# Kernel tuning notes

Measured on AMD Instinct MI355X. Metric: run time of the kernel, lower is better.

The kernel has to match this reference:

```python
import jax, jax.numpy as jnp
import numpy as np

E = 2048  # embed_size == seq_len (required: edge_weight_fc maps last dim E -> 1 on the NxN scores)
B = 4
N = 2048


def setup_inputs() -> dict:
    key = jax.random.key(0)
    ks = jax.random.split(key, 12)
    s = 0.02
    inp = {
        "query": jax.random.normal(ks[0], (B, N, E), jnp.float32),
        "key": jax.random.normal(ks[1], (B, N, E), jnp.float32),
        "value": jax.random.normal(ks[2], (B, N, E), jnp.float32),
        "mask": jax.random.randint(ks[3], (B, N, N), 0, 2, jnp.int32),
        # nn.Linear weights stored torch-style as [out, in]
        "Wq": jax.random.normal(ks[4], (E, E), jnp.float32) * s,
        "bq": jnp.zeros((E,), jnp.float32),
        "Wk": jax.random.normal(ks[5], (E, E), jnp.float32) * s,
        "bk": jnp.zeros((E,), jnp.float32),
        "Wv": jax.random.normal(ks[6], (E, E), jnp.float32) * s,
        "bv": jnp.zeros((E,), jnp.float32),
        "We": jax.random.normal(ks[7], (1, E), jnp.float32) * s,  # edge_weight_fc: Linear(E, 1)
        "be": jnp.zeros((1,), jnp.float32),
        "Wo": jax.random.normal(ks[8], (E, E), jnp.float32) * s,
        "bo": jnp.zeros((E,), jnp.float32),
    }
    return inp


def reference(query, key, value, mask, Wq, bq, Wk, bk, Wv, bv, We, be, Wo, bo):
    # QKV projections (torch Linear: x @ W.T + b)
    Q = query @ Wq.T + bq                       # [B, N, E]
    K = key @ Wk.T + bk                         # [B, N, E]
    V = value @ Wv.T + bv                       # [B, N, E]
    scale = 1.0 / jnp.sqrt(jnp.asarray(E, jnp.float32))
    scores = jnp.einsum("bqe,bke->bqk", Q, K) * scale   # [B, N, N]
    scores = scores + mask.astype(scores.dtype) * (-1e9)
    # graph_structure is non-None -> learned sigmoid edge gate over score rows
    edge_w = jax.nn.sigmoid(scores @ We.T + be)          # [B, N, 1]
    scores = scores * edge_w
    attn = jax.nn.softmax(scores, axis=-1)               # [B, N, N]
    # dropout is identity in eval mode
    out = jnp.einsum("bqk,bke->bqe", attn, V)            # [B, N, E]
    return out @ Wo.T + bo
```

## Files before the change

### kernel.cpp

```cpp
#include <hip/hip_runtime.h>
#include <math.h>

#define BB 4
#define NN 2048
#define EE 2048

typedef __attribute__((ext_vector_type(8))) unsigned short ushort8;
typedef __attribute__((ext_vector_type(8))) __bf16 bf16x8;
typedef __attribute__((ext_vector_type(4))) float f32x4;

__device__ __forceinline__ unsigned short f2bf(float f) {
  unsigned int u = __float_as_uint(f);
  u = u + 0x7fffu + ((u >> 16) & 1u);
  return (unsigned short)(u >> 16);
}
__device__ __forceinline__ float bf2f(unsigned short h) {
  return __uint_as_float((unsigned)h << 16);
}

__device__ __forceinline__ void gload16(const void* g, void* l) {
  __builtin_amdgcn_global_load_lds(
      (__attribute__((address_space(1))) void*)g,
      (__attribute__((address_space(3))) void*)l, 16, 0, 0);
}

#define SCHED_FENCE() __builtin_amdgcn_sched_barrier(0)
#define BARRIER() do { SCHED_FENCE(); __builtin_amdgcn_s_barrier(); SCHED_FENCE(); } while (0)
#define WAIT_VM(N) do { SCHED_FENCE(); asm volatile("s_waitcnt vmcnt(" #N ")"); SCHED_FENCE(); } while (0)

__global__ __launch_bounds__(256) void k_f32_to_bf16(const float* __restrict__ in,
                                                     unsigned short* __restrict__ out) {
  size_t i = (size_t)blockIdx.x * 256 + threadIdx.x;
  const float4* ip = (const float4*)in;
  float4 a = ip[i * 2];
  float4 b = ip[i * 2 + 1];
  ushort8 o;
  o[0] = f2bf(a.x); o[1] = f2bf(a.y); o[2] = f2bf(a.z); o[3] = f2bf(a.w);
  o[4] = f2bf(b.x); o[5] = f2bf(b.y); o[6] = f2bf(b.z); o[7] = f2bf(b.w);
  *((ushort8*)out + i) = o;
}

__global__ __launch_bounds__(256) void k_trf2b(const float* __restrict__ in,
                                               unsigned short* __restrict__ out) {
  __shared__ __attribute__((aligned(16))) unsigned short tile[64][72];
  const long eb = (long)blockIdx.x * 64;
  const long nb = (long)blockIdx.y * 64;
  const int t = threadIdx.x;
  const int r = t >> 3;
  const int c = (t & 7) * 8;

  const float* p0 = in + (nb + r) * (long)EE + eb + c;
  const float* p1 = in + (nb + 32 + r) * (long)EE + eb + c;
  float4 a0 = *(const float4*)p0, a1 = *(const float4*)(p0 + 4);
  float4 b0 = *(const float4*)p1, b1 = *(const float4*)(p1 + 4);
  unsigned short* t0 = &tile[r][c];
  unsigned short* t1 = &tile[r + 32][c];
  t0[0] = f2bf(a0.x); t0[1] = f2bf(a0.y); t0[2] = f2bf(a0.z); t0[3] = f2bf(a0.w);
  t0[4] = f2bf(a1.x); t0[5] = f2bf(a1.y); t0[6] = f2bf(a1.z); t0[7] = f2bf(a1.w);
  t1[0] = f2bf(b0.x); t1[1] = f2bf(b0.y); t1[2] = f2bf(b0.z); t1[3] = f2bf(b0.w);
  t1[4] = f2bf(b1.x); t1[5] = f2bf(b1.y); t1[6] = f2bf(b1.z); t1[7] = f2bf(b1.w);
  __syncthreads();
  ushort8 o0, o1;
#pragma unroll
  for (int j = 0; j < 8; j++) { o0[j] = tile[c + j][r]; o1[j] = tile[c + j][r + 32]; }
  *(ushort8*)(out + (eb + r) * (long)NN + nb + c) = o0;
  *(ushort8*)(out + (eb + r + 32) * (long)NN + nb + c) = o1;
}

__global__ __launch_bounds__(256) void k_transpose(const unsigned short* __restrict__ in,
                                                   unsigned short* __restrict__ out) {
  __shared__ __attribute__((aligned(16))) unsigned short tile[64][72];
  const long z = blockIdx.z;
  const long eb = (long)blockIdx.x * 64;
  const long nb = (long)blockIdx.y * 64;
  const unsigned short* ip = in + z * (long)NN * EE;
  unsigned short* op = out + z * (long)NN * EE;
  const int t = threadIdx.x;
  const int r = t >> 3;
  const int c = (t & 7) * 8;

  ushort8 u0 = *(const ushort8*)(ip + (nb + r) * EE + eb + c);
  ushort8 u1 = *(const ushort8*)(ip + (nb + 32 + r) * EE + eb + c);
  *(ushort8*)&tile[r][c] = u0;
  *(ushort8*)&tile[r + 32][c] = u1;
  __syncthreads();
  ushort8 o0, o1;
#pragma unroll
  for (int j = 0; j < 8; j++) { o0[j] = tile[c + j][r]; o1[j] = tile[c + j][r + 32]; }
  *(ushort8*)(op + (eb + r) * NN + nb + c) = o0;
  *(ushort8*)(op + (eb + r + 32) * NN + nb + c) = o1;
}

__global__ __launch_bounds__(256) void k_vecw(const float* __restrict__ Wq,
                                              const float* __restrict__ Wk,
                                              const float* __restrict__ bq,
                                              const float* __restrict__ bk,
                                              float* __restrict__ u,
                                              float* __restrict__ w2b,
                                              float* __restrict__ t4) {
  const int e = blockIdx.x * 256 + threadIdx.x;
  const int tt0 = blockIdx.y * 64;
  float su = 0.f, sw = 0.f;
#pragma unroll 4
  for (int i = 0; i < 64; i++) {
    int tt = tt0 + i;
    su += Wq[(long)tt * EE + e] * bk[tt];
    sw += Wk[(long)tt * EE + e] * bq[tt];
  }
  atomicAdd(&u[e], su);
  atomicAdd(&w2b[e], sw);
  if (blockIdx.x == 0 && threadIdx.x < 64) {
    int lane = threadIdx.x;
    float p = bq[tt0 + lane] * bk[tt0 + lane];
    for (int off = 32; off >= 1; off >>= 1) p += __shfl_down(p, off);
    if (lane == 0) atomicAdd(t4, p);
  }
}

__global__ __launch_bounds__(256) void k_cvec(const float* __restrict__ Wo,
                                              const float* __restrict__ bv,
                                              const float* __restrict__ bo,
                                              float* __restrict__ cv) {
  int row = blockIdx.x * 4 + (threadIdx.x >> 6);
  int lane = threadIdx.x & 63;
  float s = 0.f;
  for (int j = lane; j < EE; j += 64) s += Wo[(long)row * EE + j] * bv[j];
  for (int off = 32; off >= 1; off >>= 1) s += __shfl_down(s, off);
  if (lane == 0) cv[row] = s + bo[row];
}

__global__ __launch_bounds__(256) void k_rowterm(const unsigned short* __restrict__ qb,
                                                 const float* __restrict__ u,
                                                 const float* __restrict__ t4,
                                                 float* __restrict__ rt) {
  long row = (long)blockIdx.x * 4 + (threadIdx.x >> 6);
  int lane = threadIdx.x & 63;
  const unsigned short* qr = qb + row * EE;
  float s = 0.f;
#pragma unroll
  for (int it = 0; it < 4; ++it) {
    int e0 = it * 512 + lane * 8;
    ushort8 qv = *(const ushort8*)(qr + e0);
#pragma unroll
    for (int j = 0; j < 8; j++) s += bf2f(qv[j]) * u[e0 + j];
  }
  for (int off = 32; off >= 1; off >>= 1) s += __shfl_down(s, off);
  if (lane == 0) rt[row] = s + *t4;
}

__global__ __launch_bounds__(512, 4) void k_gemm128(
    const unsigned short* __restrict__ A, long lda, long sA,
    const unsigned short* __restrict__ Bm, long ldb, long sB,
    unsigned short* __restrict__ Co, long ldc, long sC, int K) {
  __shared__ __attribute__((aligned(16))) unsigned short As[2 * 8192];
  __shared__ __attribute__((aligned(16))) unsigned short Bs[2 * 8192];
  const int gx = gridDim.x, gy = gridDim.y;
  int lin = (int)blockIdx.x + gx * ((int)blockIdx.y + gy * (int)blockIdx.z);
  int nwg = gx * gy * (int)gridDim.z;
  int chunk = nwg >> 3;
  int sw = (lin & 7) * chunk + (lin >> 3);
  int bz = sw / (gx * gy); int rem = sw - bz * (gx * gy);
  int by = rem / gx; int bx = rem - by * gx;

  const long m0 = (long)by * 128;
  const long n0 = (long)bx * 128;
  const unsigned short* Ab = A + (long)bz * sA;
  const unsigned short* Bb = Bm + (long)bz * sB;
  const int t = threadIdx.x;
  const int lane = t & 63;
  const int w = t >> 6;
  const int wm = w >> 2, wn = w & 3;

  const int srow = t >> 3;
  const int scol = (((t & 7) * 16) ^ (((t >> 5) & 1) << 5)) >> 1;
  const unsigned short* Ga = Ab + (m0 + srow) * lda + scol;
  const unsigned short* Gb = Bb + (n0 + srow) * ldb + scol;
  const int ldst = t * 8;

#define STAGE(buf, tile) do { \
    const unsigned short* ga_ = Ga + (long)(tile) * 64; \
    const unsigned short* gb_ = Gb + (long)(tile) * 64; \
    unsigned short* la_ = As + (buf) * 8192 + ldst; \
    unsigned short* lb_ = Bs + (buf) * 8192 + ldst; \
    gload16(ga_, la_); gload16(ga_ + 64 * lda, la_ + 4096); \
    gload16(gb_, lb_); gload16(gb_ + 64 * ldb, lb_ + 4096); \
  } while (0)

  const int r = lane & 15;
  const int q = lane >> 4;
  const int rb2 = ((r * 128 + q * 16) ^ ((r & 4) << 3)) >> 1;
  const int aBase = wm * 4096 + rb2;
  const int bBase = wn * 2048 + rb2;

  f32x4 acc[4][2] = {};
  bf16x8 a[4][2], b[2][2];
  const int J = K >> 6;
  STAGE(0, 0);
  WAIT_VM(0);
  BARRIER();
  for (int j = 0; j < J; ++j) {
    const int c = j & 1;
    const unsigned short* Ac = As + c * 8192;
    const unsigned short* Bc = Bs + c * 8192;
#pragma unroll
    for (int mi = 0; mi < 4; mi++)
#pragma unroll
      for (int kk = 0; kk < 2; kk++)
        a[mi][kk] = *(const bf16x8*)(Ac + aBase + mi * 1024 + kk * 32);
#pragma unroll
    for (int ni = 0; ni < 2; ni++)
#pragma unroll
      for (int kk = 0; kk < 2; kk++)
        b[ni][kk] = *(const bf16x8*)(Bc + bBase + ni * 1024 + kk * 32);
    if (j + 1 < J) STAGE(c ^ 1, j + 1);
    __builtin_amdgcn_s_setprio(1);
#pragma unroll
    for (int mi = 0; mi < 4; mi++)
#pragma unroll
      for (int ni = 0; ni < 2; ni++)
#pragma unroll
        for (int kk = 0; kk < 2; kk++)
          acc[mi][ni] = __builtin_amdgcn_mfma_f32_16x16x32_bf16(
              a[mi][kk], b[ni][kk], acc[mi][ni], 0, 0, 0);
    __builtin_amdgcn_s_setprio(0);
    WAIT_VM(0);
    BARRIER();
  }
#undef STAGE
  const int cr0 = wm * 64 + (q << 2);
  const int cc0 = wn * 32 + r;
#pragma unroll
  for (int mi = 0; mi < 4; mi++)
#pragma unroll
    for (int rr = 0; rr < 4; rr++) {
      long row = m0 + cr0 + mi * 16 + rr;
#pragma unroll
      for (int ni = 0; ni < 2; ni++)
        Co[(long)bz * sC + row * ldc + n0 + cc0 + ni * 16] = f2bf(acc[mi][ni][rr]);
    }
}

template <int EPI>
__global__ __launch_bounds__(512, 2) void k_gemm256(
    const unsigned short* __restrict__ A, long lda, long sA,
    const unsigned short* __restrict__ Bm, long ldb, long sB,
    void* __restrict__ Cv, long ldc, long sC, int K,
    const float* __restrict__ bias,
    const int* __restrict__ mask, long sMask,
    const float* __restrict__ rt, float scale,
    const float* __restrict__ We, float* __restrict__ edot) {
  __shared__ __attribute__((aligned(16))) unsigned short As[2 * 16384];
  __shared__ __attribute__((aligned(16))) unsigned short Bs[2 * 16384];

  const int gx = gridDim.x, gy = gridDim.y;
  int lin = (int)blockIdx.x + gx * ((int)blockIdx.y + gy * (int)blockIdx.z);
  int nwg = gx * gy * (int)gridDim.z;
  int chunk = nwg >> 3;
  int sw = (lin & 7) * chunk + (lin >> 3);
  int bz = sw / (gx * gy); int rem = sw - bz * (gx * gy);
  int by = rem / gx; int bx = rem - by * gx;

  const long m0 = (long)by * 256;
  const long n0 = (long)bx * 256;
  const unsigned short* Ab = A + (long)bz * sA;
  const unsigned short* Bb = Bm + (long)bz * sB;

  const int t = threadIdx.x;
  const int lane = t & 63;
  const int w = t >> 6;
  const int wm = w >> 2;
  const int wn = w & 3;

  const int p0 = t * 16;
  const int q0 = p0 ^ (((p0 >> 9) & 1) << 5);
  const int srow = ((q0 >> 10) >> 1) * 16 + ((q0 >> 6) & 15);
  const int scol = ((q0 >> 10) & 1) * 32 + ((q0 & 63) >> 1);
  const unsigned short* Ga = Ab + (m0 + srow) * lda + scol;
  const unsigned short* Gb = Bb + (n0 + srow) * ldb + scol;
  const int ldst = t * 8;

#define STAGE_A(buf, h, tile) do { \
    const unsigned short* g_ = Ga + (long)(tile) * 64 + (long)(h) * 128 * lda; \
    unsigned short* l_ = As + (buf) * 16384 + (h) * 8192 + ldst; \
    gload16(g_, l_); gload16(g_ + 64 * lda, l_ + 4096); \
  } while (0)
#define STAGE_B(buf, h, tile) do { \
    const unsigned short* g_ = Gb + (long)(tile) * 64 + (long)(h) * 128 * ldb; \
    unsigned short* l_ = Bs + (buf) * 16384 + (h) * 8192 + ldst; \
    gload16(g_, l_); gload16(g_ + 64 * ldb, l_ + 4096); \
  } while (0)

  const int r = lane & 15;
  const int q = lane >> 4;
  const int c2h = ((q * 16) ^ (((lane >> 3) & 1) << 5)) >> 1;
  const int aBase = wm * 8192 + r * 32 + c2h;
  const int bBase = (wn >> 1) * 8192 + (wn & 1) * 4096 + r * 32 + c2h;

#define RD_A(bp, mbase) do { \
    _Pragma("unroll") for (int mi = 0; mi < 4; mi++) \
    _Pragma("unroll") for (int kk = 0; kk < 2; kk++) \
      a[mi][kk] = *(const bf16x8*)((bp) + aBase + ((mbase) + mi) * 1024 + kk * 512); \
  } while (0)
#define RD_B(bp, nbase) do { \
    _Pragma("unroll") for (int ni = 0; ni < 2; ni++) \
    _Pragma("unroll") for (int kk = 0; kk < 2; kk++) \
      b[(nbase) + ni][kk] = *(const bf16x8*)((bp) + bBase + ((nbase) + ni) * 1024 + kk * 512); \
  } while (0)
#define MFMA_Q(mbase, nbase) do { \
    BARRIER(); \
    __builtin_amdgcn_s_setprio(1); \
    _Pragma("unroll") for (int mi = 0; mi < 4; mi++) \
    _Pragma("unroll") for (int ni = 0; ni < 2; ni++) \
    _Pragma("unroll") for (int kk = 0; kk < 2; kk++) \
      acc[(mbase) + mi][(nbase) + ni] = __builtin_amdgcn_mfma_f32_16x16x32_bf16( \
          a[mi][kk], b[(nbase) + ni][kk], acc[(mbase) + mi][(nbase) + ni], 0, 0, 0); \
    __builtin_amdgcn_s_setprio(0); \
    BARRIER(); \
  } while (0)

  f32x4 acc[8][4] = {};
  bf16x8 a[4][2], b[4][2];
  const unsigned short* A0 = As;
  const unsigned short* B0 = Bs;
  const unsigned short* A1 = As + 16384;
  const unsigned short* B1 = Bs + 16384;
  const int J = K >> 7;

  STAGE_B(0, 0, 0); STAGE_B(0, 1, 0);
  STAGE_A(0, 0, 0); STAGE_A(0, 1, 0);
  STAGE_B(1, 0, 1); STAGE_B(1, 1, 1);
  WAIT_VM(4);
  BARRIER();

  for (int j = 0; j < J; ++j) {
    const int t0 = 2 * j, t1 = 2 * j + 1;
    const bool pf = (j + 1 < J);

    RD_A(A0, 0); RD_B(B0, 0);
    STAGE_A(1, 0, t1);
    MFMA_Q(0, 0);

    RD_B(B0, 2);
    STAGE_A(1, 1, t1);
    MFMA_Q(0, 2);

    RD_A(A0, 4);
    if (pf) STAGE_B(0, 0, t0 + 2);
    MFMA_Q(4, 0);

    if (pf) { STAGE_B(0, 1, t0 + 2); WAIT_VM(4); } else { WAIT_VM(0); }
    MFMA_Q(4, 2);

    RD_A(A1, 0); RD_B(B1, 0);
    if (pf) STAGE_A(0, 0, t0 + 2);
    MFMA_Q(0, 0);

    RD_B(B1, 2);
    if (pf) STAGE_A(0, 1, t0 + 2);
    MFMA_Q(0, 2);

    RD_A(A1, 4);
    if (pf) STAGE_B(1, 0, t1 + 2);
    MFMA_Q(4, 0);

    if (pf) { STAGE_B(1, 1, t1 + 2); WAIT_VM(4); }
    MFMA_Q(4, 2);
  }
#undef STAGE_A
#undef STAGE_B
#undef RD_A
#undef RD_B
#undef MFMA_Q

  const int cr0 = wm * 128 + (q << 2);
  const int cc0 = wn * 64 + r;
  if (EPI == 0) {
    unsigned short* Co = (unsigned short*)Cv + (long)bz * sC;
#pragma unroll
    for (int mi = 0; mi < 8; mi++)
#pragma unroll
      for (int rr = 0; rr < 4; rr++) {
        long row = m0 + cr0 + mi * 16 + rr;
#pragma unroll
        for (int ni = 0; ni < 4; ni++) {
          long col = n0 + cc0 + ni * 16;
          float v = acc[mi][ni][rr];
          if (bias) v += bias[col];
          Co[row * ldc + col] = f2bf(v);
        }
      }
  } else if (EPI == 1) {
    unsigned short* Co = (unsigned short*)Cv + (long)bz * sC;
    const int* Mp = mask + (long)bz * sMask;
    const float* rtb = rt + (long)bz * NN;
    float* edpart = (float*)As;
    if (t < 256) edpart[t] = 0.f;
    __syncthreads();
    float wec[4];
#pragma unroll
    for (int ni = 0; ni < 4; ni++) wec[ni] = We[n0 + cc0 + ni * 16];
#pragma unroll
    for (int mi = 0; mi < 8; mi++) {
      float pr[4];
#pragma unroll
      for (int rr = 0; rr < 4; rr++) {
        long row = m0 + cr0 + mi * 16 + rr;
        float rv = rtb[row];
        float pv = 0.f;
#pragma unroll
        for (int ni = 0; ni < 4; ni++) {
          long col = n0 + cc0 + ni * 16;
          float sm = (acc[mi][ni][rr] + rv) * scale + (float)Mp[row * ldc + col] * -1e9f;
          Co[row * ldc + col] = f2bf(sm);
          pv += sm * wec[ni];
        }
        pr[rr] = pv;
      }
#pragma unroll
      for (int mask_ = 1; mask_ < 16; mask_ <<= 1)
#pragma unroll
        for (int rr = 0; rr < 4; rr++) pr[rr] += __shfl_xor(pr[rr], mask_);
      if (r == 0) {
#pragma unroll
        for (int rr = 0; rr < 4; rr++)
          atomicAdd(&edpart[cr0 + mi * 16 + rr], pr[rr]);
      }
    }
    __syncthreads();
    if (t < 256) atomicAdd(&edot[(long)bz * NN + m0 + t], edpart[t]);
  } else {
    float* Co = (float*)Cv + (long)bz * sC;
#pragma unroll
    for (int mi = 0; mi < 8; mi++)
#pragma unroll
      for (int rr = 0; rr < 4; rr++) {
        long row = m0 + cr0 + mi * 16 + rr;
#pragma unroll
        for (int ni = 0; ni < 4; ni++) {
          long col = n0 + cc0 + ni * 16;
          Co[row * ldc + col] = acc[mi][ni][rr] + bias[col];
        }
      }
  }
}

__global__ __launch_bounds__(256) void k_edge_softmax(unsigned short* __restrict__ attn,
                                                      const float* __restrict__ edot,
                                                      const float* __restrict__ be) {
  __shared__ float r2[4], r3[4];
  const long row = blockIdx.x;
  unsigned short* srow = attn + row * (long)NN;
  const int t = threadIdx.x;
  const int lane = t & 63;
  const int w = t >> 6;

  float edge = 1.0f / (1.0f + expf(-(edot[row] + be[0])));
  ushort8 v = *(const ushort8*)(srow + t * 8);
  float s[8];
  float mx = -3.4e38f;
#pragma unroll
  for (int j = 0; j < 8; j++) { s[j] = bf2f(v[j]) * edge; mx = fmaxf(mx, s[j]); }
#pragma unroll
  for (int off = 32; off >= 1; off >>= 1) mx = fmaxf(mx, __shfl_down(mx, off));
  if (lane == 0) r2[w] = mx;
  __syncthreads();
  mx = fmaxf(fmaxf(r2[0], r2[1]), fmaxf(r2[2], r2[3]));

  float sum = 0.f;
  float p[8];
#pragma unroll
  for (int j = 0; j < 8; j++) { p[j] = expf(s[j] - mx); sum += p[j]; }
#pragma unroll
  for (int off = 32; off >= 1; off >>= 1) sum += __shfl_down(sum, off);
  if (lane == 0) r3[w] = sum;
  __syncthreads();
  sum = r3[0] + r3[1] + r3[2] + r3[3];
  float inv = 1.0f / sum;

  ushort8 o;
#pragma unroll
  for (int j = 0; j < 8; j++) o[j] = f2bf(p[j] * inv);
  *(ushort8*)(srow + t * 8) = o;
}

extern "C" void kernel_launch(void* const* d_in, const int* in_sizes, int n_in,
                              void* d_out, int out_size, void* d_ws, size_t ws_size,
                              hipStream_t stream) {
  (void)in_sizes; (void)n_in; (void)out_size; (void)ws_size;
  const float* query = (const float*)d_in[0];
  const float* key_  = (const float*)d_in[1];
  const float* value = (const float*)d_in[2];
  const int*   mask  = (const int*)d_in[3];
  const float* Wq = (const float*)d_in[4];
  const float* bq = (const float*)d_in[5];
  const float* Wk = (const float*)d_in[6];
  const float* bk = (const float*)d_in[7];
  const float* Wv = (const float*)d_in[8];
  const float* bv = (const float*)d_in[9];
  const float* We = (const float*)d_in[10];
  const float* be = (const float*)d_in[11];
  const float* Wo = (const float*)d_in[12];
  const float* bo = (const float*)d_in[13];
  float* out = (float*)d_out;

  const long WSZ = (long)EE * EE;
  char* ws = (char*)d_ws;
  unsigned short* WkT = (unsigned short*)(ws);
  unsigned short* Wob = WkT + WSZ;
  unsigned short* WqT = WkT + 2 * WSZ;
  unsigned short* WvT = WkT + 3 * WSZ;
  unsigned short* W2T = (unsigned short*)(ws + 33554432L);
  unsigned short* W3T = W2T + WSZ;
  unsigned short* attn = (unsigned short*)(ws);
  unsigned short* qb  = (unsigned short*)(ws + 79691776L);
  unsigned short* kb  = (unsigned short*)(ws + 114294784L);
  unsigned short* vb  = (unsigned short*)(ws + 148897792L);
  unsigned short* Tb  = vb;
  unsigned short* Vt2 = (unsigned short*)(ws + 183500800L);
  unsigned short* Vt2T = qb;
  float* cvec = (float*)(ws + 219938816L);
  float* uvec = cvec + EE;
  float* w2b  = cvec + 2 * EE;
  float* t4   = cvec + 3 * EE;
  float* rt   = cvec + 3 * EE + 64;
  float* edot = rt + (long)BB * NN;

  const float scale = 1.0f / sqrtf((float)EE);
  dim3 blk(256), blk5(512);

  k_trf2b<<<dim3(32, 32), blk, 0, stream>>>(Wk, WkT);
  k_trf2b<<<dim3(32, 32), blk, 0, stream>>>(Wq, WqT);
  k_trf2b<<<dim3(32, 32), blk, 0, stream>>>(Wv, WvT);
  k_f32_to_bf16<<<2048, blk, 0, stream>>>(Wo, Wob);
  hipMemsetAsync(uvec, 0, (2 * EE + 64) * sizeof(float), stream);
  hipMemsetAsync(edot, 0, (long)BB * NN * sizeof(float), stream);
  k_vecw<<<dim3(8, 32), blk, 0, stream>>>(Wq, Wk, bq, bk, uvec, w2b, t4);
  k_cvec<<<512, blk, 0, stream>>>(Wo, bv, bo, cvec);
  k_gemm128<<<dim3(16, 16, 2), blk5, 0, stream>>>(WkT, EE, WSZ, WqT, EE, WSZ,
      W2T, EE, WSZ, EE);
  k_f32_to_bf16<<<8192, blk, 0, stream>>>(query, qb);
  k_f32_to_bf16<<<8192, blk, 0, stream>>>(key_, kb);
  k_f32_to_bf16<<<8192, blk, 0, stream>>>(value, vb);
  k_gemm256<0><<<dim3(8, 32, 1), blk5, 0, stream>>>(vb, EE, 0, W3T, EE, 0,
      Vt2, EE, 0, EE, nullptr, nullptr, 0, nullptr, 0.f, nullptr, nullptr);
  k_gemm256<0><<<dim3(8, 32, 1), blk5, 0, stream>>>(qb, EE, 0, W2T, EE, 0,
      Tb, EE, 0, EE, w2b, nullptr, 0, nullptr, 0.f, nullptr, nullptr);
  k_rowterm<<<2048, blk, 0, stream>>>(qb, uvec, t4, rt);
  k_transpose<<<dim3(32, 32, BB), blk, 0, stream>>>(Vt2, Vt2T);
  k_gemm256<1><<<dim3(8, 8, BB), blk5, 0, stream>>>(Tb, EE, (long)NN * EE, kb, EE, (long)NN * EE,
      attn, NN, (long)NN * NN, EE, nullptr, mask, (long)NN * NN, rt, scale, We, edot);
  k_edge_softmax<<<BB * NN, blk, 0, stream>>>(attn, edot, be);
  k_gemm256<2><<<dim3(8, 8, BB), blk5, 0, stream>>>(attn, NN, (long)NN * NN,
      Vt2T, NN, (long)EE * NN, out, EE, (long)NN * EE, NN,
      cvec, nullptr, 0, nullptr, 0.f, nullptr, nullptr);
}
```

Baseline: 482.0 us.

## Switch GEMM inner loop from 16x16x32 to 32x32x16 bf16 MFMA tiles

```diff
diff --git a/kernel.cpp b/kernel.cpp
--- a/kernel.cpp
+++ b/kernel.cpp
@@ -8,6 +8,7 @@
 typedef __attribute__((ext_vector_type(8))) unsigned short ushort8;
 typedef __attribute__((ext_vector_type(8))) __bf16 bf16x8;
 typedef __attribute__((ext_vector_type(4))) float f32x4;
+typedef __attribute__((ext_vector_type(16))) float f32x16;
 
 __device__ __forceinline__ unsigned short f2bf(float f) {
   unsigned int u = __float_as_uint(f);
@@ -290,36 +291,38 @@
     gload16(g_, l_); gload16(g_ + 64 * ldb, l_ + 4096); \
   } while (0)
 
-  const int r = lane & 15;
-  const int q = lane >> 4;
-  const int c2h = ((q * 16) ^ (((lane >> 3) & 1) << 5)) >> 1;
-  const int aBase = wm * 8192 + r * 32 + c2h;
-  const int bBase = (wn >> 1) * 8192 + (wn & 1) * 4096 + r * 32 + c2h;
-
-#define RD_A(bp, mbase) do { \
-    _Pragma("unroll") for (int mi = 0; mi < 4; mi++) \
-    _Pragma("unroll") for (int kk = 0; kk < 2; kk++) \
-      a[mi][kk] = *(const bf16x8*)((bp) + aBase + ((mbase) + mi) * 1024 + kk * 512); \
+  const int rA = lane & 15;
+  const int sg = (lane >> 4) & 1;
+  const int k8 = lane >> 5;
+  const int xr = (rA >> 3) & 1;
+  const int laneRK = rA * 32 + k8 * 8;
+  const int aHalf = wm * 8192;
+  const int bHalf = (wn >> 1) * 8192 + (wn & 1) * 4096;
+
+#define RD_A2(bp, mp) do { \
+    _Pragma("unroll") for (int mi = 0; mi < 2; mi++) \
+    _Pragma("unroll") for (int ks = 0; ks < 4; ks++) \
+      a[mi][ks] = *(const bf16x8*)((bp) + aHalf + ((((mp) + mi) * 2 + sg) * 2 + (ks >> 1)) * 512 \
+                                   + laneRK + ((((ks & 1) ^ xr)) << 4)); \
   } while (0)
-#define RD_B(bp, nbase) do { \
-    _Pragma("unroll") for (int ni = 0; ni < 2; ni++) \
-    _Pragma("unroll") for (int kk = 0; kk < 2; kk++) \
-      b[(nbase) + ni][kk] = *(const bf16x8*)((bp) + bBase + ((nbase) + ni) * 1024 + kk * 512); \
+#define RD_B2(bp, nj) do { \
+    _Pragma("unroll") for (int ks = 0; ks < 4; ks++) \
+      b[nj][ks] = *(const bf16x8*)((bp) + bHalf + (((nj) * 2 + sg) * 2 + (ks >> 1)) * 512 \
+                                   + laneRK + ((((ks & 1) ^ xr)) << 4)); \
   } while (0)
-#define MFMA_Q(mbase, nbase) do { \
+#define MFMA_W(mb, nj) do { \
     BARRIER(); \
     __builtin_amdgcn_s_setprio(1); \
-    _Pragma("unroll") for (int mi = 0; mi < 4; mi++) \
-    _Pragma("unroll") for (int ni = 0; ni < 2; ni++) \
-    _Pragma("unroll") for (int kk = 0; kk < 2; kk++) \
-      acc[(mbase) + mi][(nbase) + ni] = __builtin_amdgcn_mfma_f32_16x16x32_bf16( \
-          a[mi][kk], b[(nbase) + ni][kk], acc[(mbase) + mi][(nbase) + ni], 0, 0, 0); \
+    _Pragma("unroll") for (int mi = 0; mi < 2; mi++) \
+    _Pragma("unroll") for (int ks = 0; ks < 4; ks++) \
+      acc[(mb) + mi][nj] = __builtin_amdgcn_mfma_f32_32x32x16_bf16( \
+          a[mi][ks], b[nj][ks], acc[(mb) + mi][nj], 0, 0, 0); \
     __builtin_amdgcn_s_setprio(0); \
     BARRIER(); \
   } while (0)
 
-  f32x4 acc[8][4] = {};
-  bf16x8 a[4][2], b[4][2];
+  f32x16 acc[4][2] = {};
+  bf16x8 a[2][4], b[2][4];
   const unsigned short* A0 = As;
   const unsigned short* B0 = Bs;
   const unsigned short* A1 = As + 16384;
@@ -336,55 +339,55 @@
     const int t0 = 2 * j, t1 = 2 * j + 1;
     const bool pf = (j + 1 < J);
 
-    RD_A(A0, 0); RD_B(B0, 0);
+    RD_A2(A0, 0); RD_B2(B0, 0);
     STAGE_A(1, 0, t1);
-    MFMA_Q(0, 0);
-
-    RD_B(B0, 2);
+    MFMA_W(0, 0);
+
+    RD_B2(B0, 1);
     STAGE_A(1, 1, t1);
-    MFMA_Q(0, 2);
-
-    RD_A(A0, 4);
+    MFMA_W(0, 1);
+
+    RD_A2(A0, 2);
     if (pf) STAGE_B(0, 0, t0 + 2);
-    MFMA_Q(4, 0);
+    MFMA_W(2, 0);
 
     if (pf) { STAGE_B(0, 1, t0 + 2); WAIT_VM(4); } else { WAIT_VM(0); }
-    MFMA_Q(4, 2);
-
-    RD_A(A1, 0); RD_B(B1, 0);
+    MFMA_W(2, 1);
+
+    RD_A2(A1, 0); RD_B2(B1, 0);
     if (pf) STAGE_A(0, 0, t0 + 2);
-    MFMA_Q(0, 0);
-
-    RD_B(B1, 2);
+    MFMA_W(0, 0);
+
+    RD_B2(B1, 1);
     if (pf) STAGE_A(0, 1, t0 + 2);
-    MFMA_Q(0, 2);
-
-    RD_A(A1, 4);
+    MFMA_W(0, 1);
+
+    RD_A2(A1, 2);
     if (pf) STAGE_B(1, 0, t1 + 2);
-    MFMA_Q(4, 0);
+    MFMA_W(2, 0);
 
     if (pf) { STAGE_B(1, 1, t1 + 2); WAIT_VM(4); }
-    MFMA_Q(4, 2);
+    MFMA_W(2, 1);
   }
 #undef STAGE_A
 #undef STAGE_B
-#undef RD_A
-#undef RD_B
-#undef MFMA_Q
-
-  const int cr0 = wm * 128 + (q << 2);
-  const int cc0 = wn * 64 + r;
+#undef RD_A2
+#undef RD_B2
+#undef MFMA_W
+
+  const int l31 = lane & 31;
+  const int q32 = lane >> 5;
   if (EPI == 0) {
     unsigned short* Co = (unsigned short*)Cv + (long)bz * sC;
 #pragma unroll
-    for (int mi = 0; mi < 8; mi++)
-#pragma unroll
-      for (int rr = 0; rr < 4; rr++) {
-        long row = m0 + cr0 + mi * 16 + rr;
-#pragma unroll
-        for (int ni = 0; ni < 4; ni++) {
-          long col = n0 + cc0 + ni * 16;
-          float v = acc[mi][ni][rr];
+    for (int mi = 0; mi < 4; mi++)
+#pragma unroll
+      for (int reg = 0; reg < 16; reg++) {
+        long row = m0 + wm * 128 + mi * 32 + (reg & 3) + 8 * (reg >> 2) + 4 * q32;
+#pragma unroll
+        for (int nj = 0; nj < 2; nj++) {
+          long col = n0 + wn * 64 + nj * 32 + l31;
+          float v = acc[mi][nj][reg];
           if (bias) v += bias[col];
           Co[row * ldc + col] = f2bf(v);
         }
@@ -396,34 +399,34 @@
     float* edpart = (float*)As;
     if (t < 256) edpart[t] = 0.f;
     __syncthreads();
-    float wec[4];
-#pragma unroll
-    for (int ni = 0; ni < 4; ni++) wec[ni] = We[n0 + cc0 + ni * 16];
-#pragma unroll
-    for (int mi = 0; mi < 8; mi++) {
-      float pr[4];
-#pragma unroll
-      for (int rr = 0; rr < 4; rr++) {
-        long row = m0 + cr0 + mi * 16 + rr;
+    float wec[2];
+#pragma unroll
+    for (int nj = 0; nj < 2; nj++) wec[nj] = We[n0 + wn * 64 + nj * 32 + l31];
+#pragma unroll
+    for (int mi = 0; mi < 4; mi++) {
+      float pv[16];
+#pragma unroll
+      for (int reg = 0; reg < 16; reg++) {
+        long row = m0 + wm * 128 + mi * 32 + (reg & 3) + 8 * (reg >> 2) + 4 * q32;
         float rv = rtb[row];
-        float pv = 0.f;
-#pragma unroll
-        for (int ni = 0; ni < 4; ni++) {
-          long col = n0 + cc0 + ni * 16;
-          float sm = (acc[mi][ni][rr] + rv) * scale + (float)Mp[row * ldc + col] * -1e9f;
+        float p = 0.f;
+#pragma unroll
+        for (int nj = 0; nj < 2; nj++) {
+          long col = n0 + wn * 64 + nj * 32 + l31;
+          float sm = (acc[mi][nj][reg] + rv) * scale + (float)Mp[row * ldc + col] * -1e9f;
           Co[row * ldc + col] = f2bf(sm);
-          pv += sm * wec[ni];
+          p += sm * wec[nj];
         }
-        pr[rr] = pv;
+        pv[reg] = p;
       }
 #pragma unroll
-      for (int mask_ = 1; mask_ < 16; mask_ <<= 1)
-#pragma unroll
-        for (int rr = 0; rr < 4; rr++) pr[rr] += __shfl_xor(pr[rr], mask_);
-      if (r == 0) {
-#pragma unroll
-        for (int rr = 0; rr < 4; rr++)
-          atomicAdd(&edpart[cr0 + mi * 16 + rr], pr[rr]);
+      for (int mask_ = 1; mask_ < 32; mask_ <<= 1)
+#pragma unroll
+        for (int reg = 0; reg < 16; reg++) pv[reg] += __shfl_xor(pv[reg], mask_);
+      if (l31 == 0) {
+#pragma unroll
+        for (int reg = 0; reg < 16; reg++)
+          atomicAdd(&edpart[wm * 128 + mi * 32 + (reg & 3) + 8 * (reg >> 2) + 4 * q32], pv[reg]);
       }
     }
     __syncthreads();
@@ -431,14 +434,14 @@
   } else {
     float* Co = (float*)Cv + (long)bz * sC;
 #pragma unroll
-    for (int mi = 0; mi < 8; mi++)
-#pragma unroll
-      for (int rr = 0; rr < 4; rr++) {
-        long row = m0 + cr0 + mi * 16 + rr;
-#pragma unroll
-        for (int ni = 0; ni < 4; ni++) {
-          long col = n0 + cc0 + ni * 16;
-          Co[row * ldc + col] = acc[mi][ni][rr] + bias[col];
+    for (int mi = 0; mi < 4; mi++)
+#pragma unroll
+      for (int reg = 0; reg < 16; reg++) {
+        long row = m0 + wm * 128 + mi * 32 + (reg & 3) + 8 * (reg >> 2) + 4 * q32;
+#pragma unroll
+        for (int nj = 0; nj < 2; nj++) {
+          long col = n0 + wn * 64 + nj * 32 + l31;
+          Co[row * ldc + col] = acc[mi][nj][reg] + bias[col];
         }
       }
   }
```

After: 525.2 us. +9.0%, slower.
